# Optimization experiments

Measured on AMD Instinct MI355X. Metric: run time of the kernel, lower is better.

The kernel has to match this reference:

```python
import jax, jax.numpy as jnp
import numpy as np

NEG_SLOPE = 0.2
EPS = 1e-16


def gat_layer(x, src, dst, W, att_src, att_dst, bias, heads, concat):
    N = x.shape[0]
    C = W.shape[1] // heads
    h = (x @ W).reshape(N, heads, C)                      # [N,H,C]
    a_src = (h * att_src).sum(-1)                         # [N,H]
    a_dst = (h * att_dst).sum(-1)                         # [N,H]
    e = jax.nn.leaky_relu(a_src[src] + a_dst[dst], NEG_SLOPE)  # [E,H]
    # numerically-stable softmax over incoming edges of each dst node
    e_max = jax.ops.segment_max(e, dst, num_segments=N)   # [N,H]
    e_max = jnp.where(jnp.isfinite(e_max), e_max, 0.0)
    ex = jnp.exp(e - e_max[dst])                          # [E,H]
    denom = jax.ops.segment_sum(ex, dst, num_segments=N) + EPS
    alpha = ex / denom[dst]                               # [E,H]
    msg = alpha[:, :, None] * h[src]                      # [E,H,C]
    out = jax.ops.segment_sum(msg, dst, num_segments=N)   # [N,H,C]
    if concat:
        return out.reshape(N, heads * C) + bias
    return out.mean(axis=1) + bias


def setup_inputs() -> dict:
    key = jax.random.key(0)
    ks = jax.random.split(key, 12)
    N, E = 50000, 800000
    IN, HID, OUT, H = 128, 8, 40, 8
    x = jax.random.normal(ks[0], (N, IN), dtype=jnp.float32)
    edge_index = jax.random.randint(ks[1], (2, E), 0, N, dtype=jnp.int64)
    s1 = 1.0 / np.sqrt(IN)
    s2 = 1.0 / np.sqrt(HID * H)
    W1 = jax.random.normal(ks[2], (IN, H * HID), dtype=jnp.float32) * s1
    att_src1 = jax.random.normal(ks[3], (H, HID), dtype=jnp.float32) * 0.1
    att_dst1 = jax.random.normal(ks[4], (H, HID), dtype=jnp.float32) * 0.1
    bias1 = jnp.zeros((H * HID,), dtype=jnp.float32)
    W2 = jax.random.normal(ks[5], (H * HID, OUT), dtype=jnp.float32) * s2
    att_src2 = jax.random.normal(ks[6], (1, OUT), dtype=jnp.float32) * 0.1
    att_dst2 = jax.random.normal(ks[7], (1, OUT), dtype=jnp.float32) * 0.1
    bias2 = jnp.zeros((OUT,), dtype=jnp.float32)
    return {"x": x, "edge_index": edge_index,
            "W1": W1, "att_src1": att_src1, "att_dst1": att_dst1, "bias1": bias1,
            "W2": W2, "att_src2": att_src2, "att_dst2": att_dst2, "bias2": bias2}


def reference(x, edge_index, W1, att_src1, att_dst1, bias1, W2, att_src2, att_dst2, bias2):
    src, dst = edge_index[0], edge_index[1]
    # eval mode: dropout is identity
    h = gat_layer(x, src, dst, W1, att_src1, att_dst1, bias1, heads=8, concat=True)
    h = jax.nn.elu(h)
    out = gat_layer(h, src, dst, W2, att_src2, att_dst2, bias2, heads=1, concat=False)
    return out
```

## Files before the change

kernel.cpp:

```cpp
#include <hip/hip_runtime.h>
#include <math.h>

#define EPS 1e-16f
#define SLOT 64
__device__ __forceinline__ float lrelu(float v) { return v > 0.0f ? v : 0.2f * v; }

__device__ __forceinline__ unsigned short f2bf(float f) {
    unsigned u = __float_as_uint(f);
    u += 0x7FFF + ((u >> 16) & 1);
    return (unsigned short)(u >> 16);
}
__device__ __forceinline__ float bf2f(unsigned short s) {
    return __uint_as_float(((unsigned)s) << 16);
}

#define LDK1 129
#define LDN1 65
__global__ __launch_bounds__(256, 2) void k_gemm1_scat(
    const float* __restrict__ x, const float* __restrict__ W1,
    const float* __restrict__ att_src1, const float* __restrict__ att_dst1,
    unsigned short* __restrict__ h1b, float* __restrict__ a_src1, float* __restrict__ a_dst1,
    int N, int D, const int* __restrict__ src, const int* __restrict__ dst,
    int* __restrict__ deg, int* __restrict__ ssrc, int E) {
    __shared__ float sX[64 * LDK1];
    __shared__ float sW[128 * LDN1];
    int t = threadIdx.x;
    if (blockIdx.x < D) {
        int e0 = (blockIdx.x * 256 + t) * 8;
        if (e0 < E) {
            int4 sa = *((const int4*)(src + e0));
            int4 sb = *((const int4*)(src + e0 + 4));
            int4 da = *((const int4*)(dst + e0));
            int4 db = *((const int4*)(dst + e0 + 4));
            int p0 = atomicAdd(&deg[da.x], 1);
            int p1 = atomicAdd(&deg[da.y], 1);
            int p2 = atomicAdd(&deg[da.z], 1);
            int p3 = atomicAdd(&deg[da.w], 1);
            int p4 = atomicAdd(&deg[db.x], 1);
            int p5 = atomicAdd(&deg[db.y], 1);
            int p6 = atomicAdd(&deg[db.z], 1);
            int p7 = atomicAdd(&deg[db.w], 1);
            if (p0 < SLOT) ssrc[(da.x << 6) + p0] = sa.x;
            if (p1 < SLOT) ssrc[(da.y << 6) + p1] = sa.y;
            if (p2 < SLOT) ssrc[(da.z << 6) + p2] = sa.z;
            if (p3 < SLOT) ssrc[(da.w << 6) + p3] = sa.w;
            if (p4 < SLOT) ssrc[(db.x << 6) + p4] = sb.x;
            if (p5 < SLOT) ssrc[(db.y << 6) + p5] = sb.y;
            if (p6 < SLOT) ssrc[(db.z << 6) + p6] = sb.z;
            if (p7 < SLOT) ssrc[(db.w << 6) + p7] = sb.w;
        }
        return;
    }
    int r0 = (blockIdx.x - D) * 64;
    for (int i = t; i < 2048; i += 256) {
        int k = i >> 4, n4 = i & 15;
        float4 v = ((const float4*)W1)[i];
        float* p = sW + k * LDN1 + 4 * n4;
        p[0] = v.x; p[1] = v.y; p[2] = v.z; p[3] = v.w;
    }
    for (int i = t; i < 2048; i += 256) {
        int m = i >> 5, k4 = i & 31;
        int r = r0 + m;
        float4 v = make_float4(0.f, 0.f, 0.f, 0.f);
        if (r < N) v = ((const float4*)(x + (size_t)r * 128))[k4];
        float* p = sX + m * LDK1 + 4 * k4;
        p[0] = v.x; p[1] = v.y; p[2] = v.z; p[3] = v.w;
    }
    __syncthreads();
    int tx = t & 15, ty = t >> 4;
    const float* pA = sX + 4 * tx * LDK1;
    const float* pB = sW + 4 * ty;
    float c[4][4] = {{0.f}};
#pragma unroll 8
    for (int k = 0; k < 128; k++) {
        float a0 = pA[k], a1 = pA[LDK1 + k], a2 = pA[2 * LDK1 + k], a3 = pA[3 * LDK1 + k];
        const float* pb = pB + k * LDN1;
        float b0 = pb[0], b1 = pb[1], b2 = pb[2], b3 = pb[3];
        c[0][0] = fmaf(a0, b0, c[0][0]); c[0][1] = fmaf(a0, b1, c[0][1]);
        c[0][2] = fmaf(a0, b2, c[0][2]); c[0][3] = fmaf(a0, b3, c[0][3]);
        c[1][0] = fmaf(a1, b0, c[1][0]); c[1][1] = fmaf(a1, b1, c[1][1]);
        c[1][2] = fmaf(a1, b2, c[1][2]); c[1][3] = fmaf(a1, b3, c[1][3]);
        c[2][0] = fmaf(a2, b0, c[2][0]); c[2][1] = fmaf(a2, b1, c[2][1]);
        c[2][2] = fmaf(a2, b2, c[2][2]); c[2][3] = fmaf(a2, b3, c[2][3]);
        c[3][0] = fmaf(a3, b0, c[3][0]); c[3][1] = fmaf(a3, b1, c[3][1]);
        c[3][2] = fmaf(a3, b2, c[3][2]); c[3][3] = fmaf(a3, b3, c[3][3]);
    }
    float as0 = att_src1[4 * ty + 0], as1 = att_src1[4 * ty + 1],
          as2 = att_src1[4 * ty + 2], as3 = att_src1[4 * ty + 3];
    float ad0 = att_dst1[4 * ty + 0], ad1 = att_dst1[4 * ty + 1],
          ad2 = att_dst1[4 * ty + 2], ad3 = att_dst1[4 * ty + 3];
    __syncthreads();
    float* sPs = sX;
    float* sPd = sX + 64 * 17;
#pragma unroll
    for (int i = 0; i < 4; i++) {
        int row = 4 * tx + i;
        int r = r0 + row;
        if (r < N) {
            ushort4 hv;
            hv.x = f2bf(c[i][0]); hv.y = f2bf(c[i][1]);
            hv.z = f2bf(c[i][2]); hv.w = f2bf(c[i][3]);
            *((ushort4*)(h1b + (size_t)r * 64 + 4 * ty)) = hv;
        }
        sPs[row * 17 + ty] = fmaf(c[i][0], as0, fmaf(c[i][1], as1, fmaf(c[i][2], as2, c[i][3] * as3)));
        sPd[row * 17 + ty] = fmaf(c[i][0], ad0, fmaf(c[i][1], ad1, fmaf(c[i][2], ad2, c[i][3] * ad3)));
    }
    __syncthreads();
    for (int i = t; i < 512; i += 256) {
        int row = i >> 3, h = i & 7;
        int r = r0 + row;
        if (r < N) {
            a_src1[r * 8 + h] = sPs[row * 17 + 2 * h] + sPs[row * 17 + 2 * h + 1];
            a_dst1[r * 8 + h] = sPd[row * 17 + 2 * h] + sPd[row * 17 + 2 * h + 1];
        }
    }
}

__global__ __launch_bounds__(256) void k_node_agg1(
    const int* __restrict__ deg, const int* __restrict__ ssrc,
    const float* __restrict__ a_src1, const float* __restrict__ a_dst1,
    const unsigned short* __restrict__ h1b, const float* __restrict__ bias1,
    float* __restrict__ xx, int N) {
    int d = (blockIdx.x * 256 + threadIdx.x) >> 6;
    int lane = threadIdx.x & 63;
    if (d >= N) return;
    int start = d << 6;
    int m = min(deg[d], SLOT);
    int h8 = lane & 7;
    int eoff = lane >> 3;
    int q = lane & 31;
    int hsel = q >> 2;
    int sub = lane >> 5;
    float adst8 = a_dst1[d * 8 + h8];
    int s_lane = 0;
    if (lane < m) s_lane = ssrc[start + lane];
    int nch = (m + 7) >> 3;
    unsigned rA[4];
#pragma unroll
    for (int k = 0; k < 4; k++) {
        int sR = __shfl(s_lane, 2 * k + sub);
        rA[k] = *((const unsigned*)(h1b + (size_t)sR * 64 + (q << 1)));
    }
    float exv[8];
    float lsumA = 0.0f;
#pragma unroll
    for (int c = 0; c < 8; c++) {
        int idx = c * 8 + eoff;
        int s_c = __shfl(s_lane, idx);
        float e = 0.0f;
        if (idx < m) e = __expf(lrelu(a_src1[(size_t)s_c * 8 + h8] + adst8));
        exv[c] = e;
        lsumA += e;
    }
    float accLo = 0.0f, accHi = 0.0f;
#pragma unroll
    for (int c = 0; c < 8; c++) {
        if (c >= nch) break;
        unsigned rB[4];
        if (c + 1 < nch) {
#pragma unroll
            for (int k = 0; k < 4; k++) {
                int sR = __shfl(s_lane, (c + 1) * 8 + 2 * k + sub);
                rB[k] = *((const unsigned*)(h1b + (size_t)sR * 64 + (q << 1)));
            }
        }
#pragma unroll
        for (int k = 0; k < 4; k++) {
            float f = __shfl(exv[c], ((2 * k + sub) << 3) | hsel);
            accLo = fmaf(f, bf2f((unsigned short)(rA[k] & 0xffff)), accLo);
            accHi = fmaf(f, bf2f((unsigned short)(rA[k] >> 16)), accHi);
        }
        if (c + 1 < nch) {
#pragma unroll
            for (int k = 0; k < 4; k++) rA[k] = rB[k];
        }
    }
    accLo += __shfl_xor(accLo, 32);
    accHi += __shfl_xor(accHi, 32);
    float t = lsumA;
    t += __shfl_xor(t, 8); t += __shfl_xor(t, 16); t += __shfl_xor(t, 32);
    float lsum = __shfl(t, hsel);
    if (lane < 32) {
        float2 bz = ((const float2*)bias1)[q];
        float oLo = accLo / (lsum + EPS) + bz.x;
        float oHi = accHi / (lsum + EPS) + bz.y;
        oLo = oLo > 0.0f ? oLo : expm1f(oLo);
        oHi = oHi > 0.0f ? oHi : expm1f(oHi);
        *((float2*)(xx + (size_t)d * 64 + 2 * q)) = make_float2(oLo, oHi);
    }
}

#define LDK2 65
#define LDN2 41
__global__ __launch_bounds__(256, 2) void k_gemm2(
    const float* __restrict__ xx, const float* __restrict__ W2,
    const float* __restrict__ att_src2, const float* __restrict__ att_dst2,
    float* __restrict__ h2, float* __restrict__ a_src2, float* __restrict__ a_dst2, int N) {
    __shared__ float sX[64 * LDK2];
    __shared__ float sW[64 * LDN2];
    int t = threadIdx.x;
    int r0 = blockIdx.x * 64;
    for (int i = t; i < 640; i += 256) {
        int k = i / 10, n4 = i - k * 10;
        float4 v = ((const float4*)W2)[i];
        float* p = sW + k * LDN2 + 4 * n4;
        p[0] = v.x; p[1] = v.y; p[2] = v.z; p[3] = v.w;
    }
    for (int i = t; i < 1024; i += 256) {
        int m = i >> 4, k4 = i & 15;
        int r = r0 + m;
        float4 v = make_float4(0.f, 0.f, 0.f, 0.f);
        if (r < N) v = ((const float4*)(xx + (size_t)r * 64))[k4];
        float* p = sX + m * LDK2 + 4 * k4;
        p[0] = v.x; p[1] = v.y; p[2] = v.z; p[3] = v.w;
    }
    __syncthreads();
    int tx = t & 15, ty = t >> 4;
    bool act = ty < 10;
    float c[4][4] = {{0.f}};
    if (act) {
        const float* pA = sX + 4 * tx * LDK2;
        const float* pB = sW + 4 * ty;
#pragma unroll 8
        for (int k = 0; k < 64; k++) {
            float a0 = pA[k], a1 = pA[LDK2 + k], a2 = pA[2 * LDK2 + k], a3 = pA[3 * LDK2 + k];
            const float* pb = pB + k * LDN2;
            float b0 = pb[0], b1 = pb[1], b2 = pb[2], b3 = pb[3];
            c[0][0] = fmaf(a0, b0, c[0][0]); c[0][1] = fmaf(a0, b1, c[0][1]);
            c[0][2] = fmaf(a0, b2, c[0][2]); c[0][3] = fmaf(a0, b3, c[0][3]);
            c[1][0] = fmaf(a1, b0, c[1][0]); c[1][1] = fmaf(a1, b1, c[1][1]);
            c[1][2] = fmaf(a1, b2, c[1][2]); c[1][3] = fmaf(a1, b3, c[1][3]);
            c[2][0] = fmaf(a2, b0, c[2][0]); c[2][1] = fmaf(a2, b1, c[2][1]);
            c[2][2] = fmaf(a2, b2, c[2][2]); c[2][3] = fmaf(a2, b3, c[2][3]);
            c[3][0] = fmaf(a3, b0, c[3][0]); c[3][1] = fmaf(a3, b1, c[3][1]);
            c[3][2] = fmaf(a3, b2, c[3][2]); c[3][3] = fmaf(a3, b3, c[3][3]);
        }
    }
    float as0 = 0.f, as1 = 0.f, as2 = 0.f, as3 = 0.f;
    float ad0 = 0.f, ad1 = 0.f, ad2 = 0.f, ad3 = 0.f;
    if (act) {
        as0 = att_src2[4 * ty + 0]; as1 = att_src2[4 * ty + 1];
        as2 = att_src2[4 * ty + 2]; as3 = att_src2[4 * ty + 3];
        ad0 = att_dst2[4 * ty + 0]; ad1 = att_dst2[4 * ty + 1];
        ad2 = att_dst2[4 * ty + 2]; ad3 = att_dst2[4 * ty + 3];
    }
    __syncthreads();
    float* sPs = sX;
    float* sPd = sX + 64 * 11;
#pragma unroll
    for (int i = 0; i < 4; i++) {
        int row = 4 * tx + i;
        int r = r0 + row;
        if (act) {
            if (r < N) {
                float4 hv = make_float4(c[i][0], c[i][1], c[i][2], c[i][3]);
                *((float4*)(h2 + (size_t)r * 40 + 4 * ty)) = hv;
            }
            sPs[row * 11 + ty] = fmaf(c[i][0], as0, fmaf(c[i][1], as1, fmaf(c[i][2], as2, c[i][3] * as3)));
            sPd[row * 11 + ty] = fmaf(c[i][0], ad0, fmaf(c[i][1], ad1, fmaf(c[i][2], ad2, c[i][3] * ad3)));
        }
    }
    __syncthreads();
    if (t < 64) {
        int r = r0 + t;
        if (r < N) {
            float ps = 0.f, pd = 0.f;
#pragma unroll
            for (int j = 0; j < 10; j++) {
                ps += sPs[t * 11 + j];
                pd += sPd[t * 11 + j];
            }
            a_src2[r] = ps;
            a_dst2[r] = pd;
        }
    }
}

__global__ __launch_bounds__(256) void k_node_agg2(
    const int* __restrict__ deg, const int* __restrict__ ssrc,
    const float* __restrict__ a_src2, const float* __restrict__ a_dst2,
    const float* __restrict__ h2, const float* __restrict__ bias2,
    float* __restrict__ out, int N) {
    int d = (blockIdx.x * 256 + threadIdx.x) >> 6;
    int lane = threadIdx.x & 63;
    if (d >= N) return;
    int start = d << 6;
    int m = min(deg[d], SLOT);
    float adst = a_dst2[d];
    int s_l = 0; float ex_l = 0.0f;
    if (lane < m) {
        s_l = ssrc[start + lane];
        ex_l = __expf(lrelu(a_src2[s_l] + adst));
    }
    int grp = lane / 20;
    int q20 = lane - grp * 20;
    bool gact = grp < 3;
    int nin = (m + 2) / 3;
    int nblk = (nin + 3) >> 2;
    float aLo = 0.0f, aHi = 0.0f;
    auto loadb = [&](int b, float2* g, float* f) {
#pragma unroll
        for (int k2 = 0; k2 < 4; k2++) {
            int j = 3 * (4 * b + k2) + grp;
            int jm = j & 63;
            int sR = __shfl(s_l, jm);
            float fv = __shfl(ex_l, jm);
            f[k2] = (gact && j < m) ? fv : 0.0f;
            g[k2] = *((const float2*)(h2 + (size_t)sR * 40 + 2 * q20));
        }
    };
    float2 gA[4]; float fA[4];
    if (nblk > 0) loadb(0, gA, fA);
#pragma unroll
    for (int b = 0; b < 6; b++) {
        if (b >= nblk) break;
        float2 gB[4]; float fB[4];
        if (b + 1 < nblk) loadb(b + 1, gB, fB);
#pragma unroll
        for (int k2 = 0; k2 < 4; k2++) {
            aLo = fmaf(fA[k2], gA[k2].x, aLo);
            aHi = fmaf(fA[k2], gA[k2].y, aHi);
        }
        if (b + 1 < nblk) {
#pragma unroll
            for (int k2 = 0; k2 < 4; k2++) { gA[k2] = gB[k2]; fA[k2] = fB[k2]; }
        }
    }
    int i1 = (lane + 20) & 63, i2 = (lane + 40) & 63;
    float ml1 = __shfl(aLo, i1), ml2 = __shfl(aLo, i2);
    float mh1 = __shfl(aHi, i1), mh2 = __shfl(aHi, i2);
    aLo += ml1 + ml2;
    aHi += mh1 + mh2;
    float t = ex_l;
#pragma unroll
    for (int off = 32; off; off >>= 1) t += __shfl_xor(t, off);
    if (lane < 20) {
        float2 bz = ((const float2*)bias2)[lane];
        float oLo = aLo / (t + EPS) + bz.x;
        float oHi = aHi / (t + EPS) + bz.y;
        *((float2*)(out + (size_t)d * 40 + 2 * lane)) = make_float2(oLo, oHi);
    }
}

extern "C" void kernel_launch(void* const* d_in, const int* in_sizes, int n_in,
                              void* d_out, int out_size, void* d_ws, size_t ws_size,
                              hipStream_t stream) {
    const float* x        = (const float*)d_in[0];
    const int*   ei       = (const int*)d_in[1];
    const float* W1       = (const float*)d_in[2];
    const float* att_src1 = (const float*)d_in[3];
    const float* att_dst1 = (const float*)d_in[4];
    const float* bias1    = (const float*)d_in[5];
    const float* W2       = (const float*)d_in[6];
    const float* att_src2 = (const float*)d_in[7];
    const float* att_dst2 = (const float*)d_in[8];
    const float* bias2    = (const float*)d_in[9];
    float* out = (float*)d_out;

    const int N = in_sizes[0] / 128;
    const int E = in_sizes[1] / 2;
    const int* src = ei;
    const int* dst = ei + E;

    float* ws = (float*)d_ws;
    size_t off = 0;
    int*   deg      = (int*)(ws + off); off += (size_t)N;
    int*   ssrc     = (int*)(ws + off); off += (size_t)N * SLOT;
    unsigned short* h1b = (unsigned short*)(ws + off); off += (size_t)N * 32;
    float* a_src1   = ws + off; off += (size_t)N * 8;
    float* a_dst1   = ws + off; off += (size_t)N * 8;
    float* xx       = ws + off; off += (size_t)N * 64;
    float* h2       = ws + off; off += (size_t)N * 40;
    float* a_src2   = ws + off; off += (size_t)N;
    float* a_dst2   = ws + off; off += (size_t)N;

    const int B = 256;
    int G1 = (N + 63) / 64;
    int D  = (E / 8 + 255) / 256;

    hipMemsetAsync(deg, 0, (size_t)N * sizeof(int), stream);
    k_gemm1_scat<<<D + G1, B, 0, stream>>>(x, W1, att_src1, att_dst1, h1b, a_src1, a_dst1,
                                           N, D, src, dst, deg, ssrc, E);
    k_node_agg1<<<(N + 3) / 4, B, 0, stream>>>(deg, ssrc, a_src1, a_dst1, h1b, bias1, xx, N);
    k_gemm2<<<G1, B, 0, stream>>>(xx, W2, att_src2, att_dst2, h2, a_src2, a_dst2, N);
    k_node_agg2<<<(N + 3) / 4, B, 0, stream>>>(deg, ssrc, a_src2, a_dst2, h2, bias2, out, N);
}
```

Measured before the change: 216.8 us.

## Split layer-1 aggregation into two half-head passes with per-lane edge logits

The layer-1 node aggregation kernel now launches twice as many blocks, and each wavefront handles one half (4 heads, 32 channels) of a destination node's features. Each lane owns one incoming edge and computes its four attention exponentials from a single float4 load, then reduces the softmax denominators with butterfly shuffles. The feature gather processes 4 edges per step across 16-lane groups, with a one-step prefetch. This is meant to raise parallelism and cut per-wave register and shuffle pressure, at the cost of reading the edge list and logits twice and issuing more, smaller gathers.

```diff
diff --git a/kernel.cpp b/kernel.cpp
--- a/kernel.cpp
+++ b/kernel.cpp
@@ -120,73 +120,70 @@
     const int* __restrict__ deg, const int* __restrict__ ssrc,
     const float* __restrict__ a_src1, const float* __restrict__ a_dst1,
     const unsigned short* __restrict__ h1b, const float* __restrict__ bias1,
-    float* __restrict__ xx, int N) {
-    int d = (blockIdx.x * 256 + threadIdx.x) >> 6;
+    float* __restrict__ xx, int N, int NB) {
+    int pass = (blockIdx.x >= NB) ? 1 : 0;
+    int nb = blockIdx.x - pass * NB;
+    int d = (nb * 256 + threadIdx.x) >> 6;
     int lane = threadIdx.x & 63;
     if (d >= N) return;
     int start = d << 6;
     int m = min(deg[d], SLOT);
-    int h8 = lane & 7;
-    int eoff = lane >> 3;
-    int q = lane & 31;
-    int hsel = q >> 2;
-    int sub = lane >> 5;
-    float adst8 = a_dst1[d * 8 + h8];
     int s_lane = 0;
     if (lane < m) s_lane = ssrc[start + lane];
-    int nch = (m + 7) >> 3;
-    unsigned rA[4];
-#pragma unroll
-    for (int k = 0; k < 4; k++) {
-        int sR = __shfl(s_lane, 2 * k + sub);
-        rA[k] = *((const unsigned*)(h1b + (size_t)sR * 64 + (q << 1)));
-    }
-    float exv[8];
-    float lsumA = 0.0f;
-#pragma unroll
-    for (int c = 0; c < 8; c++) {
-        int idx = c * 8 + eoff;
-        int s_c = __shfl(s_lane, idx);
-        float e = 0.0f;
-        if (idx < m) e = __expf(lrelu(a_src1[(size_t)s_c * 8 + h8] + adst8));
-        exv[c] = e;
-        lsumA += e;
-    }
-    float accLo = 0.0f, accHi = 0.0f;
-#pragma unroll
-    for (int c = 0; c < 8; c++) {
-        if (c >= nch) break;
-        unsigned rB[4];
-        if (c + 1 < nch) {
-#pragma unroll
-            for (int k = 0; k < 4; k++) {
-                int sR = __shfl(s_lane, (c + 1) * 8 + 2 * k + sub);
-                rB[k] = *((const unsigned*)(h1b + (size_t)sR * 64 + (q << 1)));
-            }
-        }
-#pragma unroll
-        for (int k = 0; k < 4; k++) {
-            float f = __shfl(exv[c], ((2 * k + sub) << 3) | hsel);
-            accLo = fmaf(f, bf2f((unsigned short)(rA[k] & 0xffff)), accLo);
-            accHi = fmaf(f, bf2f((unsigned short)(rA[k] >> 16)), accHi);
-        }
-        if (c + 1 < nch) {
-#pragma unroll
-            for (int k = 0; k < 4; k++) rA[k] = rB[k];
-        }
-    }
-    accLo += __shfl_xor(accLo, 32);
-    accHi += __shfl_xor(accHi, 32);
-    float t = lsumA;
-    t += __shfl_xor(t, 8); t += __shfl_xor(t, 16); t += __shfl_xor(t, 32);
-    float lsum = __shfl(t, hsel);
-    if (lane < 32) {
-        float2 bz = ((const float2*)bias1)[q];
+    float4 ad4 = *((const float4*)(a_dst1 + (size_t)d * 8 + 4 * pass));
+    float4 as4 = *((const float4*)(a_src1 + (size_t)s_lane * 8 + 4 * pass));
+    float e0 = 0.f, e1 = 0.f, e2 = 0.f, e3 = 0.f;
+    if (lane < m) {
+        e0 = __expf(lrelu(as4.x + ad4.x));
+        e1 = __expf(lrelu(as4.y + ad4.y));
+        e2 = __expf(lrelu(as4.z + ad4.z));
+        e3 = __expf(lrelu(as4.w + ad4.w));
+    }
+    float t0 = e0, t1 = e1, t2 = e2, t3 = e3;
+#pragma unroll
+    for (int off = 32; off; off >>= 1) {
+        t0 += __shfl_xor(t0, off); t1 += __shfl_xor(t1, off);
+        t2 += __shfl_xor(t2, off); t3 += __shfl_xor(t3, off);
+    }
+    int q = lane & 15;
+    int rg = lane >> 4;
+    int hsel = q >> 2;
+    int coff = 32 * pass + 2 * q;
+    int nblk = (m + 3) >> 2;
+    float accLo = 0.f, accHi = 0.f;
+    unsigned rA = 0; float fA = 0.f;
+    {
+        int sR = __shfl(s_lane, rg);
+        rA = *((const unsigned*)(h1b + (size_t)sR * 64 + coff));
+        float c0 = __shfl(e0, rg), c1 = __shfl(e1, rg), c2 = __shfl(e2, rg), c3 = __shfl(e3, rg);
+        fA = hsel == 0 ? c0 : hsel == 1 ? c1 : hsel == 2 ? c2 : c3;
+    }
+#pragma unroll
+    for (int jb = 0; jb < 16; jb++) {
+        if (jb >= nblk) break;
+        unsigned rB = 0; float fB = 0.f;
+        if (jb + 1 < nblk) {
+            int eidx = (jb + 1) * 4 + rg;
+            int sR = __shfl(s_lane, eidx);
+            rB = *((const unsigned*)(h1b + (size_t)sR * 64 + coff));
+            float c0 = __shfl(e0, eidx), c1 = __shfl(e1, eidx);
+            float c2 = __shfl(e2, eidx), c3 = __shfl(e3, eidx);
+            fB = hsel == 0 ? c0 : hsel == 1 ? c1 : hsel == 2 ? c2 : c3;
+        }
+        accLo = fmaf(fA, bf2f((unsigned short)(rA & 0xffff)), accLo);
+        accHi = fmaf(fA, bf2f((unsigned short)(rA >> 16)), accHi);
+        rA = rB; fA = fB;
+    }
+    accLo += __shfl_xor(accLo, 16); accHi += __shfl_xor(accHi, 16);
+    accLo += __shfl_xor(accLo, 32); accHi += __shfl_xor(accHi, 32);
+    float lsum = hsel == 0 ? t0 : hsel == 1 ? t1 : hsel == 2 ? t2 : t3;
+    if (lane < 16) {
+        float2 bz = ((const float2*)(bias1 + 32 * pass))[q];
         float oLo = accLo / (lsum + EPS) + bz.x;
         float oHi = accHi / (lsum + EPS) + bz.y;
         oLo = oLo > 0.0f ? oLo : expm1f(oLo);
         oHi = oHi > 0.0f ? oHi : expm1f(oHi);
-        *((float2*)(xx + (size_t)d * 64 + 2 * q)) = make_float2(oLo, oHi);
+        *((float2*)(xx + (size_t)d * 64 + 32 * pass + 2 * q)) = make_float2(oLo, oHi);
     }
 }
 
@@ -377,11 +374,12 @@
     const int B = 256;
     int G1 = (N + 63) / 64;
     int D  = (E / 8 + 255) / 256;
+    int NB = (N + 3) / 4;
 
     hipMemsetAsync(deg, 0, (size_t)N * sizeof(int), stream);
     k_gemm1_scat<<<D + G1, B, 0, stream>>>(x, W1, att_src1, att_dst1, h1b, a_src1, a_dst1,
                                            N, D, src, dst, deg, ssrc, E);
-    k_node_agg1<<<(N + 3) / 4, B, 0, stream>>>(deg, ssrc, a_src1, a_dst1, h1b, bias1, xx, N);
+    k_node_agg1<<<2 * NB, B, 0, stream>>>(deg, ssrc, a_src1, a_dst1, h1b, bias1, xx, N, NB);
     k_gemm2<<<G1, B, 0, stream>>>(xx, W2, att_src2, att_dst2, h2, a_src2, a_dst2, N);
     k_node_agg2<<<(N + 3) / 4, B, 0, stream>>>(deg, ssrc, a_src2, a_dst2, h2, bias2, out, N);
 }
```

Result: slower. 244.7 us (+12.9%).
